# Kernel tuning notes

Measured on AMD Instinct MI355X. Metric: run time of the kernel, lower is better.

## Reference

```python
import jax, jax.numpy as jnp
import numpy as np

B, N, F, H = 2, 2048, 1024, 16
HD = F // H
SQRT_D = float(np.sqrt(F))  # note: module scales by sqrt(in_c), not sqrt(head_dim)


def setup_inputs() -> dict:
    key = jax.random.key(0)
    ks = jax.random.split(key, 9)
    s = 1.0 / np.sqrt(F)
    mk = lambda k: jax.random.uniform(k, (F, F), jnp.float32, -s, s)
    mb = lambda k: jax.random.uniform(k, (F,), jnp.float32, -s, s)
    return {
        "x": jax.random.normal(ks[0], (B, N, F), jnp.float32),
        "Wq": mk(ks[1]), "bq": mb(ks[2]),
        "Wk": mk(ks[3]), "bk": mb(ks[4]),
        "Wv": mk(ks[5]), "bv": mb(ks[6]),
        "Wo": mk(ks[7]), "bo": mb(ks[8]),
    }


def reference(x, Wq, bq, Wk, bk, Wv, bv, Wo, bo):
    b, n, f = x.shape
    # projections (torch Linear: x @ W.T + b); view to (b, n, h, hd)
    q = (x @ Wq.T + bq).reshape(b, n, H, HD)
    k = (x @ Wk.T + bk).reshape(b, n, H, HD)
    v = (x @ Wv.T + bv).reshape(b, n, H, HD)
    score = jnp.einsum('bihd,bjhd->bhij', q, k)
    attn = jax.nn.softmax(score / SQRT_D, axis=-1)
    o = jnp.einsum('bhij,bjhd->bihd', attn, v).reshape(b, n, f)
    return o @ Wo.T + bo
```

## Files before the change

### kernel.cpp

```cpp
#include <hip/hip_runtime.h>
#include <hip/hip_bf16.h>
#include <stdint.h>
#include <stddef.h>

typedef __bf16 bf16;
typedef __attribute__((ext_vector_type(8))) __bf16 bf16x8;
typedef __attribute__((ext_vector_type(4))) __bf16 bf16x4;
typedef __attribute__((ext_vector_type(2))) __bf16 bf16x2;
typedef __attribute__((ext_vector_type(4))) float f32x4;

#define MFMA16(a, b, c) __builtin_amdgcn_mfma_f32_16x16x32_bf16(a, b, c, 0, 0, 0)

#define BB 2
#define SEQ 2048
#define FDIM 1024
#define NH 16
#define HD 64
#define M_TOK 4096
#define N_QKV 3072

#define CSC 0.04508422f

__device__ __forceinline__ void gll16(const bf16* g, bf16* l) {
    __builtin_amdgcn_global_load_lds(
        (const __attribute__((address_space(1))) void*)g,
        (__attribute__((address_space(3))) void*)l, 16, 0, 0);
}

__device__ __forceinline__ bf16 pack_bf16(float f) {
    uint32_t u = __builtin_bit_cast(uint32_t, f);
    uint16_t h = (uint16_t)((u + 0x8000u) >> 16);
    return __builtin_bit_cast(bf16, h);
}

__device__ __forceinline__ uint32_t pk2(float a, float b) {
#if __has_builtin(__builtin_amdgcn_cvt_pk_bf16_f32)
    bf16x2 t = __builtin_amdgcn_cvt_pk_bf16_f32(a, b);
    return __builtin_bit_cast(uint32_t, t);
#else
    uint32_t ua = __builtin_bit_cast(uint32_t, a) + 0x8000u;
    uint32_t ub = __builtin_bit_cast(uint32_t, b) + 0x8000u;
    return __builtin_amdgcn_perm(ub, ua, 0x07060302);
#endif
}

__global__ __launch_bounds__(256) void convert_k(
    const float* __restrict__ x,
    const float* __restrict__ Wq, const float* __restrict__ bq,
    const float* __restrict__ Wk, const float* __restrict__ bk,
    const float* __restrict__ Wv, const float* __restrict__ bv,
    const float* __restrict__ Wo,
    bf16* __restrict__ xb, bf16* __restrict__ Wcat, bf16* __restrict__ Wob,
    float* __restrict__ bcat)
{
    const int tid = blockIdx.x * blockDim.x + threadIdx.x;
    const int nt = gridDim.x * blockDim.x;
    const int NX4 = M_TOK * FDIM / 4;
    const int NW4 = FDIM * FDIM / 4;

    for (int i = tid; i < NX4; i += nt) {
        float4 v = ((const float4*)x)[i];
        bf16x4 o; o[0] = (bf16)v.x; o[1] = (bf16)v.y; o[2] = (bf16)v.z; o[3] = (bf16)v.w;
        ((bf16x4*)xb)[i] = o;
    }
    for (int i = tid; i < NW4; i += nt) {
        float4 v = ((const float4*)Wq)[i];
        bf16x4 o;
        o[0] = (bf16)(v.x * CSC); o[1] = (bf16)(v.y * CSC);
        o[2] = (bf16)(v.z * CSC); o[3] = (bf16)(v.w * CSC);
        ((bf16x4*)Wcat)[i] = o;
        v = ((const float4*)Wk)[i];
        o[0] = (bf16)v.x; o[1] = (bf16)v.y; o[2] = (bf16)v.z; o[3] = (bf16)v.w;
        ((bf16x4*)Wcat)[NW4 + i] = o;
        v = ((const float4*)Wv)[i];
        o[0] = (bf16)v.x; o[1] = (bf16)v.y; o[2] = (bf16)v.z; o[3] = (bf16)v.w;
        ((bf16x4*)Wcat)[2 * NW4 + i] = o;
        v = ((const float4*)Wo)[i];
        o[0] = (bf16)v.x; o[1] = (bf16)v.y; o[2] = (bf16)v.z; o[3] = (bf16)v.w;
        ((bf16x4*)Wob)[i] = o;
    }
    for (int i = tid; i < FDIM; i += nt) {
        bcat[i] = bq[i] * CSC;
        bcat[FDIM + i] = bk[i];
        bcat[2 * FDIM + i] = bv[i];
    }
}

__global__ __launch_bounds__(512, 2) void gemm256(
    const bf16* __restrict__ A,
    const bf16* __restrict__ Bw,
    const float* __restrict__ bias,
    bf16* __restrict__ Cb,
    bf16* __restrict__ VtOut,
    int M, int N, int K)
{
    extern __shared__ char smem[];
    const int tid = threadIdx.x;
    const int lane = tid & 63;
    const int wave = tid >> 6;
    const int wr = wave >> 2;
    const int wc = wave & 3;
    const int m0 = blockIdx.y * 256;
    const int n0 = blockIdx.x * 256;
    const int lrow = lane & 15;
    const int quad = lane >> 4;
    const int NT = K >> 6;

    const int l8 = lane >> 3;
    const int kx = ((lane & 7) ^ l8) << 3;
    const int lcl = wave * 16 + l8;

#define ASTG(sl, kt, mh, c) do { \
    const int _lc = lcl + (c) * 8; \
    const int _gr = m0 + ((_lc >> 6) << 7) + ((mh) << 6) + (_lc & 63); \
    gll16(A + (size_t)_gr * K + (size_t)(kt) * 64 + kx, \
          (bf16*)(smem + (sl) * 65536 + (mh) * 16384 + wave * 2048 + (c) * 1024)); \
} while (0)
#define BSTG(sl, kt, nh, c) do { \
    const int _lc = lcl + (c) * 8; \
    const int _gc = n0 + ((_lc >> 5) << 6) + ((nh) << 5) + (_lc & 31); \
    gll16(Bw + (size_t)_gc * K + (size_t)(kt) * 64 + kx, \
          (bf16*)(smem + (sl) * 65536 + 32768 + (nh) * 16384 + wave * 2048 + (c) * 1024)); \
} while (0)

    const int swz0 = ((quad ^ (lrow & 7)) << 4);
    const int swz1 = (((4 + quad) ^ (lrow & 7)) << 4);
    const int arow = (wr * 64 + lrow) * 128;
    const int brow = (wc * 32 + lrow) * 128;

    f32x4 acc[8][4] = {};
    bf16x8 af[4][2];
    bf16x8 bc[2][2][2];

    ASTG(0, 0, 0, 0); ASTG(0, 0, 0, 1);
    BSTG(0, 0, 0, 0); BSTG(0, 0, 0, 1);
    BSTG(0, 0, 1, 0); BSTG(0, 0, 1, 1);
    ASTG(0, 0, 1, 0); ASTG(0, 0, 1, 1);
    asm volatile("s_waitcnt vmcnt(4)" ::: "memory");
    __builtin_amdgcn_s_barrier();

    for (int t = 0; t < NT; ++t) {
        const int sl = t & 1;
        const int ns = sl ^ 1;
        const char* sb = smem + sl * 65536;
        const bool pf = (t + 1 < NT);

#pragma unroll
        for (int ph = 0; ph < 4; ++ph) {
            const int mh = ph >> 1, nh = ph & 1;
            if (pf) {
                if (ph == 0)      { ASTG(ns, t + 1, 0, 0); ASTG(ns, t + 1, 0, 1); }
                else if (ph == 1) { BSTG(ns, t + 1, 0, 0); BSTG(ns, t + 1, 0, 1); }
                else if (ph == 2) { BSTG(ns, t + 1, 1, 0); BSTG(ns, t + 1, 1, 1); }
                else              { ASTG(ns, t + 1, 1, 0); ASTG(ns, t + 1, 1, 1); }
            }
            if (nh == 0) {
#pragma unroll
                for (int iq = 0; iq < 4; ++iq) {
                    af[iq][0] = *(const bf16x8*)(sb + mh * 16384 + arow + iq * 2048 + swz0);
                    af[iq][1] = *(const bf16x8*)(sb + mh * 16384 + arow + iq * 2048 + swz1);
                }
            }
            if (ph == 0 || ph == 1) {
#pragma unroll
                for (int jq = 0; jq < 2; ++jq) {
                    bc[nh][jq][0] = *(const bf16x8*)(sb + 32768 + nh * 16384 + brow + jq * 2048 + swz0);
                    bc[nh][jq][1] = *(const bf16x8*)(sb + 32768 + nh * 16384 + brow + jq * 2048 + swz1);
                }
            }
            __builtin_amdgcn_s_setprio(1);
#pragma unroll
            for (int iq = 0; iq < 4; ++iq)
#pragma unroll
                for (int jq = 0; jq < 2; ++jq) {
                    acc[mh * 4 + iq][nh * 2 + jq] =
                        MFMA16(af[iq][0], bc[nh][jq][0], acc[mh * 4 + iq][nh * 2 + jq]);
                    acc[mh * 4 + iq][nh * 2 + jq] =
                        MFMA16(af[iq][1], bc[nh][jq][1], acc[mh * 4 + iq][nh * 2 + jq]);
                }
            __builtin_amdgcn_s_setprio(0);
            if (pf) asm volatile("s_waitcnt vmcnt(4)" ::: "memory");
            else    asm volatile("s_waitcnt vmcnt(0)" ::: "memory");
            __builtin_amdgcn_s_barrier();
        }
    }
#undef ASTG
#undef BSTG

    if (VtOut && n0 >= 2048) {
        const int bql = (m0 >> 11);
#pragma unroll
        for (int i = 0; i < 8; ++i) {
#pragma unroll
            for (int j = 0; j < 4; ++j) {
                const int col = n0 + wc * 64 + (j >> 1) * 32 + (j & 1) * 16 + lrow;
                const float bsv = bias[col];
                const int vh = col - 2048;
                const int row = m0 + wr * 128 + (i >> 2) * 64 + (i & 3) * 16 + quad * 4;
                const int jj = row & (SEQ - 1);
                const int g = jj & 63;
                const int jj2 = (jj & ~63) | ((g >> 5) << 5)
                              | (((g >> 2) & 3) << 3) | (((g >> 4) & 1) << 2);
                bf16x4 vv;
#pragma unroll
                for (int r = 0; r < 4; ++r)
                    vv[r] = pack_bf16(acc[i][j][r] + bsv);
                *(bf16x4*)&VtOut[((size_t)bql * 16 * 64 + vh) * SEQ + jj2] = vv;
            }
        }
        return;
    }
#pragma unroll
    for (int i = 0; i < 8; ++i) {
#pragma unroll
        for (int j = 0; j < 4; ++j) {
            const int col = n0 + wc * 64 + (j >> 1) * 32 + (j & 1) * 16 + lrow;
            const float bsv = bias[col];
#pragma unroll
            for (int r = 0; r < 4; ++r) {
                const int row = m0 + wr * 128 + (i >> 2) * 64 + (i & 3) * 16 + quad * 4 + r;
                Cb[(size_t)row * N + col] = pack_bf16(acc[i][j][r] + bsv);
            }
        }
    }
}

__global__ __launch_bounds__(512, 2) void gemm128(
    const bf16* __restrict__ A,
    const bf16* __restrict__ Bw,
    const float* __restrict__ bias,
    float* __restrict__ Cf,
    int M, int N, int K)
{
    extern __shared__ char smem[];
    const int tid = threadIdx.x;
    const int lane = tid & 63;
    const int wave = tid >> 6;
    const int wr = wave >> 2;
    const int wc = wave & 3;
    const int m0 = blockIdx.y * 128;
    const int n0 = blockIdx.x * 128;
    const int lrow = lane & 15;
    const int quad = lane >> 4;
    const int NT = K >> 6;

    const int l8 = lane >> 3;
    const int kx = ((lane & 7) ^ l8) << 3;

#define ASTG(sl, kt, c) do { \
    const int _gr = m0 + (c) * 64 + wave * 8 + l8; \
    gll16(A + (size_t)_gr * K + (size_t)(kt) * 64 + kx, \
          (bf16*)(smem + (sl) * 32768 + (c) * 8192 + wave * 1024)); \
} while (0)
#define BSTG(sl, kt, c) do { \
    const int _gc = n0 + (c) * 64 + wave * 8 + l8; \
    gll16(Bw + (size_t)_gc * K + (size_t)(kt) * 64 + kx, \
          (bf16*)(smem + (sl) * 32768 + 16384 + (c) * 8192 + wave * 1024)); \
} while (0)

    const int swz0 = ((quad ^ (lrow & 7)) << 4);
    const int swz1 = (((4 + quad) ^ (lrow & 7)) << 4);
    const int arow0 = (wr * 32 + lrow) * 128;
    const int brow = (wc * 32 + lrow) * 128;

    f32x4 acc[4][2] = {};
    bf16x8 bfr[2][2];

    BSTG(0, 0, 0); BSTG(0, 0, 1);
    ASTG(0, 0, 0); ASTG(0, 0, 1);
    asm volatile("s_waitcnt vmcnt(1)" ::: "memory");
    __builtin_amdgcn_s_barrier();

    for (int t = 0; t < NT; ++t) {
        const int sl = t & 1;
        const int ns = sl ^ 1;
        const char* sb = smem + sl * 32768;
        const bool pf = (t + 1 < NT);

        if (pf) { BSTG(ns, t + 1, 0); BSTG(ns, t + 1, 1); }
        bf16x8 af[2][2];
#pragma unroll
        for (int jq = 0; jq < 2; ++jq) {
            bfr[jq][0] = *(const bf16x8*)(sb + 16384 + brow + jq * 2048 + swz0);
            bfr[jq][1] = *(const bf16x8*)(sb + 16384 + brow + jq * 2048 + swz1);
        }
#pragma unroll
        for (int iq = 0; iq < 2; ++iq) {
            af[iq][0] = *(const bf16x8*)(sb + arow0 + iq * 2048 + swz0);
            af[iq][1] = *(const bf16x8*)(sb + arow0 + iq * 2048 + swz1);
        }
        __builtin_amdgcn_s_setprio(1);
#pragma unroll
        for (int iq = 0; iq < 2; ++iq)
#pragma unroll
            for (int jq = 0; jq < 2; ++jq) {
                acc[iq][jq] = MFMA16(af[iq][0], bfr[jq][0], acc[iq][jq]);
                acc[iq][jq] = MFMA16(af[iq][1], bfr[jq][1], acc[iq][jq]);
            }
        __builtin_amdgcn_s_setprio(0);
        if (pf) asm volatile("s_waitcnt vmcnt(2)" ::: "memory");
        else    asm volatile("s_waitcnt vmcnt(0)" ::: "memory");
        __builtin_amdgcn_s_barrier();

        if (pf) { ASTG(ns, t + 1, 0); ASTG(ns, t + 1, 1); }
#pragma unroll
        for (int iq = 0; iq < 2; ++iq) {
            af[iq][0] = *(const bf16x8*)(sb + 8192 + arow0 + iq * 2048 + swz0);
            af[iq][1] = *(const bf16x8*)(sb + 8192 + arow0 + iq * 2048 + swz1);
        }
        __builtin_amdgcn_s_setprio(1);
#pragma unroll
        for (int iq = 0; iq < 2; ++iq)
#pragma unroll
            for (int jq = 0; jq < 2; ++jq) {
                acc[2 + iq][jq] = MFMA16(af[iq][0], bfr[jq][0], acc[2 + iq][jq]);
                acc[2 + iq][jq] = MFMA16(af[iq][1], bfr[jq][1], acc[2 + iq][jq]);
            }
        __builtin_amdgcn_s_setprio(0);
        if (pf) asm volatile("s_waitcnt vmcnt(1)" ::: "memory");
        else    asm volatile("s_waitcnt vmcnt(0)" ::: "memory");
        __builtin_amdgcn_s_barrier();
    }
#undef ASTG
#undef BSTG

#pragma unroll
    for (int iq = 0; iq < 4; ++iq) {
#pragma unroll
        for (int jq = 0; jq < 2; ++jq) {
            const int col = n0 + wc * 32 + jq * 16 + lrow;
            const float bsv = bias[col];
#pragma unroll
            for (int r = 0; r < 4; ++r) {
                const int row = m0 + (iq >> 1) * 64 + wr * 32 + (iq & 1) * 16 + quad * 4 + r;
                Cf[(size_t)row * N + col] = acc[iq][jq][r] + bsv;
            }
        }
    }
}

__global__ __launch_bounds__(512, 4) void attn_k(
    const bf16* __restrict__ QKV,
    const bf16* __restrict__ Vt,
    bf16* __restrict__ O)
{
    const int bx = blockIdx.x;
    const int bh = (bx & 7) + 8 * ((bx >> 3) & 3);
    const int qblk = bx >> 5;
    const int b = bh >> 4;
    const int h = bh & 15;
    const int lane = threadIdx.x & 63;
    const int wave = threadIdx.x >> 6;
    const int qg = wave & 3;
    const int jp = wave >> 2;
    const int lrow = lane & 15;
    const int quad = lane >> 4;
    const int lk8 = quad * 8;

    __shared__ __align__(16) bf16 Ks[2][2][128 * 32];
    __shared__ __align__(16) bf16 Vs[2][4][64 * 32];

    const size_t base = (size_t)b * SEQ * N_QKV;
    const bf16* Qp = QKV + base + h * HD;
    const bf16* Kp = QKV + base + FDIM + h * HD;
    const bf16* Vtp = Vt + (size_t)bh * HD * SEQ;

    const int qr0 = qblk * 128 + qg * 32;

    bf16x8 qf[2][2];
#pragma unroll
    for (int qt = 0; qt < 2; ++qt)
#pragma unroll
        for (int ks = 0; ks < 2; ++ks)
            qf[qt][ks] = *(const bf16x8*)(Qp + (size_t)(qr0 + qt * 16 + lrow) * N_QKV
                                          + ks * 32 + lk8);

    bf16x8 ones8;
#pragma unroll
    for (int e = 0; e < 8; ++e) ones8[e] = (bf16)1.0f;

    const f32x4 zf = {0.f, 0.f, 0.f, 0.f};

    f32x4 o[2][4] = {};
    f32x4 o4[2] = {};

    const int srow = wave * 16 + (lane >> 2);
    const int scol = ((lane & 3) ^ ((lane >> 3) & 3)) * 8;
    const bf16* kg = Kp + (size_t)srow * N_QKV + scol;
    const int vsrow = qg * 16 + (lane >> 2);
    const bf16* vg = Vtp + (size_t)vsrow * SEQ + jp * 32 + scol;
    const int kwo = wave * 512;
    const int swz8 = (quad ^ ((lrow >> 1) & 3)) * 8;

    gll16(kg,      &Ks[0][0][0] + kwo);
    gll16(kg + 32, &Ks[0][1][0] + kwo);
    gll16(vg,      &Vs[0][0][0] + kwo);
    gll16(vg + 64, &Vs[0][2][0] + kwo);
    kg += (size_t)128 * N_QKV;
    vg += 128;

    for (int jt = 0; jt < SEQ / 128; ++jt) {
        const int cur = jt & 1;
        __syncthreads();

        if (jt + 1 < SEQ / 128) {
            const int nxt = cur ^ 1;
            gll16(kg,      &Ks[nxt][0][0] + kwo);
            gll16(kg + 32, &Ks[nxt][1][0] + kwo);
            gll16(vg,      &Vs[nxt][0][0] + kwo);
            gll16(vg + 64, &Vs[nxt][2][0] + kwo);
            kg += (size_t)128 * N_QKV;
            vg += 128;
        }

#pragma unroll
        for (int pp = 0; pp < 2; ++pp) {
            const int p = (pp << 1) | jp;
            f32x4 Sp[2][2];
            __builtin_amdgcn_s_setprio(1);
#pragma unroll
            for (int m = 0; m < 2; ++m) {
                const int jn = 2 * p + m;
                bf16x8 kb0 = *(const bf16x8*)&Ks[cur][0][(jn * 16 + lrow) * 32 + swz8];
                bf16x8 kb1 = *(const bf16x8*)&Ks[cur][1][(jn * 16 + lrow) * 32 + swz8];
                Sp[m][0] = MFMA16(kb0, qf[0][0], zf);
                Sp[m][0] = MFMA16(kb1, qf[0][1], Sp[m][0]);
                Sp[m][1] = MFMA16(kb0, qf[1][0], zf);
                Sp[m][1] = MFMA16(kb1, qf[1][1], Sp[m][1]);
            }
            __builtin_amdgcn_s_setprio(0);

            union { bf16x8 v; uint32_t d[4]; } pb[2];
#pragma unroll
            for (int qt = 0; qt < 2; ++qt) {
                const f32x4 s0 = Sp[0][qt];
                const f32x4 s1 = Sp[1][qt];
                pb[qt].d[0] = pk2(__builtin_amdgcn_exp2f(s0[0]),
                                  __builtin_amdgcn_exp2f(s0[1]));
                pb[qt].d[1] = pk2(__builtin_amdgcn_exp2f(s0[2]),
                                  __builtin_amdgcn_exp2f(s0[3]));
                pb[qt].d[2] = pk2(__builtin_amdgcn_exp2f(s1[0]),
                                  __builtin_amdgcn_exp2f(s1[1]));
                pb[qt].d[3] = pk2(__builtin_amdgcn_exp2f(s1[2]),
                                  __builtin_amdgcn_exp2f(s1[3]));
            }

            __builtin_amdgcn_s_setprio(1);
            o4[0] = MFMA16(ones8, pb[0].v, o4[0]);
            o4[1] = MFMA16(ones8, pb[1].v, o4[1]);
#pragma unroll
            for (int df = 0; df < 4; ++df) {
                bf16x8 vA = *(const bf16x8*)&Vs[cur][p][(df * 16 + lrow) * 32 + swz8];
                o[0][df] = MFMA16(vA, pb[0].v, o[0][df]);
                o[1][df] = MFMA16(vA, pb[1].v, o[1][df]);
            }
            __builtin_amdgcn_s_setprio(0);
        }
    }

    __syncthreads();
    float* shO = (float*)Ks;
    float* shS = (float*)Vs;
    if (jp == 1) {
#pragma unroll
        for (int qt = 0; qt < 2; ++qt)
#pragma unroll
            for (int df = 0; df < 4; ++df)
                *(f32x4*)&shO[((((qt * 4 + df) * 4) + qg) * 64 + lane) * 4] = o[qt][df];
        shS[(qg * 64 + lane) * 2 + 0] = o4[0][0];
        shS[(qg * 64 + lane) * 2 + 1] = o4[1][0];
    }
    __syncthreads();
    if (jp == 1) return;

#pragma unroll
    for (int qt = 0; qt < 2; ++qt)
#pragma unroll
        for (int df = 0; df < 4; ++df) {
            f32x4 t = *(const f32x4*)&shO[((((qt * 4 + df) * 4) + qg) * 64 + lane) * 4];
            o[qt][df][0] += t[0]; o[qt][df][1] += t[1];
            o[qt][df][2] += t[2]; o[qt][df][3] += t[3];
        }
    const float den0 = o4[0][0] + shS[(qg * 64 + lane) * 2 + 0];
    const float den1 = o4[1][0] + shS[(qg * 64 + lane) * 2 + 1];

#pragma unroll
    for (int qt = 0; qt < 2; ++qt) {
        const float inv = 1.0f / (qt ? den1 : den0);
        const int q = qr0 + qt * 16 + lrow;
#pragma unroll
        for (int df = 0; df < 4; ++df) {
            bf16x4 vv;
#pragma unroll
            for (int r = 0; r < 4; ++r)
                vv[r] = pack_bf16(o[qt][df][r] * inv);
            *(bf16x4*)&O[(size_t)(b * SEQ + q) * FDIM + h * HD + df * 16 + quad * 4] = vv;
        }
    }
}

extern "C" void kernel_launch(void* const* d_in, const int* in_sizes, int n_in,
                              void* d_out, int out_size, void* d_ws, size_t ws_size,
                              hipStream_t stream) {
    (void)in_sizes; (void)n_in; (void)out_size; (void)ws_size;
    const float* x  = (const float*)d_in[0];
    const float* Wq = (const float*)d_in[1];
    const float* bq = (const float*)d_in[2];
    const float* Wk = (const float*)d_in[3];
    const float* bk = (const float*)d_in[4];
    const float* Wv = (const float*)d_in[5];
    const float* bv = (const float*)d_in[6];
    const float* Wo = (const float*)d_in[7];
    const float* bo = (const float*)d_in[8];
    float* out = (float*)d_out;

    char* ws = (char*)d_ws;
    bf16* xb    = (bf16*)(ws);
    bf16* Wcat  = (bf16*)(ws + 8388608);
    bf16* Wob   = (bf16*)(ws + 14680064);
    float* bcat = (float*)(ws + 16777216);
    bf16* QKV   = (bf16*)(ws + 16789504);
    bf16* Vt    = (bf16*)(ws + 41955328);
    bf16* Ob    = xb;

    static bool s_attr_done = false;
    if (!s_attr_done) {
        (void)hipFuncSetAttribute(reinterpret_cast<const void*>(gemm256),
                                  hipFuncAttributeMaxDynamicSharedMemorySize,
                                  131072);
        (void)hipFuncSetAttribute(reinterpret_cast<const void*>(gemm128),
                                  hipFuncAttributeMaxDynamicSharedMemorySize,
                                  65536);
        s_attr_done = true;
    }

    convert_k<<<dim3(1024), dim3(256), 0, stream>>>(x, Wq, bq, Wk, bk, Wv, bv, Wo,
                                                    xb, Wcat, Wob, bcat);
    gemm256<<<dim3(N_QKV / 256, M_TOK / 256), dim3(512), 131072, stream>>>(
        xb, Wcat, bcat, QKV, Vt, M_TOK, N_QKV, FDIM);
    attn_k<<<dim3((SEQ / 128) * BB * NH), dim3(512), 0, stream>>>(QKV, Vt, Ob);
    gemm128<<<dim3(FDIM / 128, M_TOK / 128), dim3(512), 65536, stream>>>(
        Ob, Wob, bo, out, M_TOK, FDIM, FDIM);
}
```

Baseline: 184.0 us.

## Retile QKV projection GEMM to 256x192 blocks with two-phase pipeline

Changes the QKV GEMM tile from 256x256 to 256x192, giving 16x16=256 blocks instead of 12x16=192. The aim is better coverage of the 256 CUs on MI355X and less wave quantization. Warp layout becomes 4x2 waves, each covering 32 rows by 96 columns per M half. The B fragments are loaded once per k-tile and reused across two A halves, and the loads are restaged in two phases. The Vt-versus-Cb epilogue choice is now made per column, since a 192-wide tile can straddle the V boundary at column 2048, which adds a branch inside the store loop. LDS use drops to 112KB.

```diff
diff --git a/kernel.cpp b/kernel.cpp
--- a/kernel.cpp
+++ b/kernel.cpp
@@ -86,7 +86,7 @@
     }
 }
 
-__global__ __launch_bounds__(512, 2) void gemm256(
+__global__ __launch_bounds__(512, 2) void gemm192(
     const bf16* __restrict__ A,
     const bf16* __restrict__ Bw,
     const float* __restrict__ bias,
@@ -98,128 +98,125 @@
     const int tid = threadIdx.x;
     const int lane = tid & 63;
     const int wave = tid >> 6;
-    const int wr = wave >> 2;
-    const int wc = wave & 3;
+    const int wr = wave >> 1;
+    const int wcn = wave & 1;
     const int m0 = blockIdx.y * 256;
-    const int n0 = blockIdx.x * 256;
+    const int n0 = blockIdx.x * 192;
     const int lrow = lane & 15;
     const int quad = lane >> 4;
     const int NT = K >> 6;
 
     const int l8 = lane >> 3;
     const int kx = ((lane & 7) ^ l8) << 3;
-    const int lcl = wave * 16 + l8;
-
-#define ASTG(sl, kt, mh, c) do { \
-    const int _lc = lcl + (c) * 8; \
-    const int _gr = m0 + ((_lc >> 6) << 7) + ((mh) << 6) + (_lc & 63); \
+
+#define ASTG(sl, kt, c) do { \
+    const int _gr = m0 + (c) * 64 + wave * 8 + l8; \
     gll16(A + (size_t)_gr * K + (size_t)(kt) * 64 + kx, \
-          (bf16*)(smem + (sl) * 65536 + (mh) * 16384 + wave * 2048 + (c) * 1024)); \
+          (bf16*)(smem + (sl) * 57344 + (c) * 8192 + wave * 1024)); \
 } while (0)
-#define BSTG(sl, kt, nh, c) do { \
-    const int _lc = lcl + (c) * 8; \
-    const int _gc = n0 + ((_lc >> 5) << 6) + ((nh) << 5) + (_lc & 31); \
+#define BSTG(sl, kt, c) do { \
+    const int _gc = n0 + (c) * 64 + wave * 8 + l8; \
     gll16(Bw + (size_t)_gc * K + (size_t)(kt) * 64 + kx, \
-          (bf16*)(smem + (sl) * 65536 + 32768 + (nh) * 16384 + wave * 2048 + (c) * 1024)); \
+          (bf16*)(smem + (sl) * 57344 + 32768 + (c) * 8192 + wave * 1024)); \
 } while (0)
 
     const int swz0 = ((quad ^ (lrow & 7)) << 4);
     const int swz1 = (((4 + quad) ^ (lrow & 7)) << 4);
-    const int arow = (wr * 64 + lrow) * 128;
-    const int brow = (wc * 32 + lrow) * 128;
-
-    f32x4 acc[8][4] = {};
-    bf16x8 af[4][2];
-    bf16x8 bc[2][2][2];
-
-    ASTG(0, 0, 0, 0); ASTG(0, 0, 0, 1);
-    BSTG(0, 0, 0, 0); BSTG(0, 0, 0, 1);
-    BSTG(0, 0, 1, 0); BSTG(0, 0, 1, 1);
-    ASTG(0, 0, 1, 0); ASTG(0, 0, 1, 1);
-    asm volatile("s_waitcnt vmcnt(4)" ::: "memory");
+    const int arow0 = (wr * 32 + lrow) * 128;
+    const int brow = (wcn * 96 + lrow) * 128;
+
+    f32x4 acc[2][2][6] = {};
+    bf16x8 bfr[6][2];
+
+    BSTG(0, 0, 0); BSTG(0, 0, 1); BSTG(0, 0, 2);
+    ASTG(0, 0, 0); ASTG(0, 0, 1);
+    ASTG(0, 0, 2); ASTG(0, 0, 3);
+    asm volatile("s_waitcnt vmcnt(2)" ::: "memory");
     __builtin_amdgcn_s_barrier();
 
     for (int t = 0; t < NT; ++t) {
         const int sl = t & 1;
         const int ns = sl ^ 1;
-        const char* sb = smem + sl * 65536;
+        const char* sb = smem + sl * 57344;
         const bool pf = (t + 1 < NT);
 
-#pragma unroll
-        for (int ph = 0; ph < 4; ++ph) {
-            const int mh = ph >> 1, nh = ph & 1;
-            if (pf) {
-                if (ph == 0)      { ASTG(ns, t + 1, 0, 0); ASTG(ns, t + 1, 0, 1); }
-                else if (ph == 1) { BSTG(ns, t + 1, 0, 0); BSTG(ns, t + 1, 0, 1); }
-                else if (ph == 2) { BSTG(ns, t + 1, 1, 0); BSTG(ns, t + 1, 1, 1); }
-                else              { ASTG(ns, t + 1, 1, 0); ASTG(ns, t + 1, 1, 1); }
-            }
-            if (nh == 0) {
-#pragma unroll
-                for (int iq = 0; iq < 4; ++iq) {
-                    af[iq][0] = *(const bf16x8*)(sb + mh * 16384 + arow + iq * 2048 + swz0);
-                    af[iq][1] = *(const bf16x8*)(sb + mh * 16384 + arow + iq * 2048 + swz1);
-                }
-            }
-            if (ph == 0 || ph == 1) {
-#pragma unroll
-                for (int jq = 0; jq < 2; ++jq) {
-                    bc[nh][jq][0] = *(const bf16x8*)(sb + 32768 + nh * 16384 + brow + jq * 2048 + swz0);
-                    bc[nh][jq][1] = *(const bf16x8*)(sb + 32768 + nh * 16384 + brow + jq * 2048 + swz1);
-                }
-            }
-            __builtin_amdgcn_s_setprio(1);
-#pragma unroll
-            for (int iq = 0; iq < 4; ++iq)
-#pragma unroll
-                for (int jq = 0; jq < 2; ++jq) {
-                    acc[mh * 4 + iq][nh * 2 + jq] =
-                        MFMA16(af[iq][0], bc[nh][jq][0], acc[mh * 4 + iq][nh * 2 + jq]);
-                    acc[mh * 4 + iq][nh * 2 + jq] =
-                        MFMA16(af[iq][1], bc[nh][jq][1], acc[mh * 4 + iq][nh * 2 + jq]);
-                }
-            __builtin_amdgcn_s_setprio(0);
-            if (pf) asm volatile("s_waitcnt vmcnt(4)" ::: "memory");
-            else    asm volatile("s_waitcnt vmcnt(0)" ::: "memory");
-            __builtin_amdgcn_s_barrier();
-        }
+        if (pf) {
+            BSTG(ns, t + 1, 0); BSTG(ns, t + 1, 1); BSTG(ns, t + 1, 2);
+            ASTG(ns, t + 1, 0); ASTG(ns, t + 1, 1);
+        }
+        bf16x8 af[2][2];
+#pragma unroll
+        for (int jf = 0; jf < 6; ++jf) {
+            bfr[jf][0] = *(const bf16x8*)(sb + 32768 + brow + jf * 2048 + swz0);
+            bfr[jf][1] = *(const bf16x8*)(sb + 32768 + brow + jf * 2048 + swz1);
+        }
+#pragma unroll
+        for (int f = 0; f < 2; ++f) {
+            af[f][0] = *(const bf16x8*)(sb + arow0 + f * 2048 + swz0);
+            af[f][1] = *(const bf16x8*)(sb + arow0 + f * 2048 + swz1);
+        }
+        __builtin_amdgcn_s_setprio(1);
+#pragma unroll
+        for (int f = 0; f < 2; ++f)
+#pragma unroll
+            for (int jf = 0; jf < 6; ++jf) {
+                acc[0][f][jf] = MFMA16(af[f][0], bfr[jf][0], acc[0][f][jf]);
+                acc[0][f][jf] = MFMA16(af[f][1], bfr[jf][1], acc[0][f][jf]);
+            }
+        __builtin_amdgcn_s_setprio(0);
+        if (pf) asm volatile("s_waitcnt vmcnt(5)" ::: "memory");
+        else    asm volatile("s_waitcnt vmcnt(0)" ::: "memory");
+        __builtin_amdgcn_s_barrier();
+
+        if (pf) { ASTG(ns, t + 1, 2); ASTG(ns, t + 1, 3); }
+#pragma unroll
+        for (int f = 0; f < 2; ++f) {
+            af[f][0] = *(const bf16x8*)(sb + 16384 + arow0 + f * 2048 + swz0);
+            af[f][1] = *(const bf16x8*)(sb + 16384 + arow0 + f * 2048 + swz1);
+        }
+        __builtin_amdgcn_s_setprio(1);
+#pragma unroll
+        for (int f = 0; f < 2; ++f)
+#pragma unroll
+            for (int jf = 0; jf < 6; ++jf) {
+                acc[1][f][jf] = MFMA16(af[f][0], bfr[jf][0], acc[1][f][jf]);
+                acc[1][f][jf] = MFMA16(af[f][1], bfr[jf][1], acc[1][f][jf]);
+            }
+        __builtin_amdgcn_s_setprio(0);
+        if (pf) asm volatile("s_waitcnt vmcnt(2)" ::: "memory");
+        else    asm volatile("s_waitcnt vmcnt(0)" ::: "memory");
+        __builtin_amdgcn_s_barrier();
     }
 #undef ASTG
 #undef BSTG
 
-    if (VtOut && n0 >= 2048) {
-        const int bql = (m0 >> 11);
-#pragma unroll
-        for (int i = 0; i < 8; ++i) {
-#pragma unroll
-            for (int j = 0; j < 4; ++j) {
-                const int col = n0 + wc * 64 + (j >> 1) * 32 + (j & 1) * 16 + lrow;
+    const int bql = (m0 >> 11);
+#pragma unroll
+    for (int mh = 0; mh < 2; ++mh) {
+#pragma unroll
+        for (int f = 0; f < 2; ++f) {
+#pragma unroll
+            for (int jf = 0; jf < 6; ++jf) {
+                const int col = n0 + wcn * 96 + jf * 16 + lrow;
                 const float bsv = bias[col];
-                const int vh = col - 2048;
-                const int row = m0 + wr * 128 + (i >> 2) * 64 + (i & 3) * 16 + quad * 4;
-                const int jj = row & (SEQ - 1);
-                const int g = jj & 63;
-                const int jj2 = (jj & ~63) | ((g >> 5) << 5)
-                              | (((g >> 2) & 3) << 3) | (((g >> 4) & 1) << 2);
-                bf16x4 vv;
-#pragma unroll
-                for (int r = 0; r < 4; ++r)
-                    vv[r] = pack_bf16(acc[i][j][r] + bsv);
-                *(bf16x4*)&VtOut[((size_t)bql * 16 * 64 + vh) * SEQ + jj2] = vv;
-            }
-        }
-        return;
-    }
-#pragma unroll
-    for (int i = 0; i < 8; ++i) {
-#pragma unroll
-        for (int j = 0; j < 4; ++j) {
-            const int col = n0 + wc * 64 + (j >> 1) * 32 + (j & 1) * 16 + lrow;
-            const float bsv = bias[col];
-#pragma unroll
-            for (int r = 0; r < 4; ++r) {
-                const int row = m0 + wr * 128 + (i >> 2) * 64 + (i & 3) * 16 + quad * 4 + r;
-                Cb[(size_t)row * N + col] = pack_bf16(acc[i][j][r] + bsv);
+                const int row = m0 + mh * 128 + wr * 32 + f * 16 + quad * 4;
+                if (VtOut && col >= 2048) {
+                    const int vh = col - 2048;
+                    const int jj = row & (SEQ - 1);
+                    const int g = jj & 63;
+                    const int jj2 = (jj & ~63) | ((g >> 5) << 5)
+                                  | (((g >> 2) & 3) << 3) | (((g >> 4) & 1) << 2);
+                    bf16x4 vv;
+#pragma unroll
+                    for (int r = 0; r < 4; ++r)
+                        vv[r] = pack_bf16(acc[mh][f][jf][r] + bsv);
+                    *(bf16x4*)&VtOut[((size_t)bql * 16 * 64 + vh) * SEQ + jj2] = vv;
+                } else {
+#pragma unroll
+                    for (int r = 0; r < 4; ++r)
+                        Cb[(size_t)(row + r) * N + col] =
+                            pack_bf16(acc[mh][f][jf][r] + bsv);
+                }
             }
         }
     }
@@ -525,9 +522,9 @@
 
     static bool s_attr_done = false;
     if (!s_attr_done) {
-        (void)hipFuncSetAttribute(reinterpret_cast<const void*>(gemm256),
+        (void)hipFuncSetAttribute(reinterpret_cast<const void*>(gemm192),
                                   hipFuncAttributeMaxDynamicSharedMemorySize,
-                                  131072);
+                                  114688);
         (void)hipFuncSetAttribute(reinterpret_cast<const void*>(gemm128),
                                   hipFuncAttributeMaxDynamicSharedMemorySize,
                                   65536);
@@ -536,7 +533,7 @@
 
     convert_k<<<dim3(1024), dim3(256), 0, stream>>>(x, Wq, bq, Wk, bk, Wv, bv, Wo,
                                                     xb, Wcat, Wob, bcat);
-    gemm256<<<dim3(N_QKV / 256, M_TOK / 256), dim3(512), 131072, stream>>>(
+    gemm192<<<dim3(N_QKV / 192, M_TOK / 256), dim3(512), 114688, stream>>>(
         xb, Wcat, bcat, QKV, Vt, M_TOK, N_QKV, FDIM);
     attn_k<<<dim3((SEQ / 128) * BB * NH), dim3(512), 0, stream>>>(QKV, Vt, Ob);
     gemm128<<<dim3(FDIM / 128, M_TOK / 128), dim3(512), 65536, stream>>>(
```

After: 180.7 us (median of 2 runs). About the same (-1.8%).

## Restructure QKV GEMM: XCD-aware block remap, new wave tiling and staging schedule

Applied to the files above, without the earlier changes.

The QKV projection GEMM now launches on a 1D grid and remaps block IDs so that consecutive blocks (which interleave across the eight XCDs) land on tiles sharing A/B panels within each XCD's L2. Each wave now holds all four B fragments for its 64-column strip once per k-tile and streams A fragments in four phases, which cuts LDS B re-reads. Global-to-LDS staging is regrouped into larger A-quarter and B-half loads, with adjusted vmcnt waits, an extra barrier and an lgkmcnt wait before the MFMAs. The extra barrier per phase adds synchronisation cost, and the output row/column mapping had to change to match the new accumulator layout.

```diff
diff --git a/kernel.cpp b/kernel.cpp
--- a/kernel.cpp
+++ b/kernel.cpp
@@ -86,7 +86,7 @@
     }
 }
 
-__global__ __launch_bounds__(512, 2) void gemm256(
+__global__ __launch_bounds__(512, 2) void gemm_qkv(
     const bf16* __restrict__ A,
     const bf16* __restrict__ Bw,
     const float* __restrict__ bias,
@@ -100,43 +100,35 @@
     const int wave = tid >> 6;
     const int wr = wave >> 2;
     const int wc = wave & 3;
-    const int m0 = blockIdx.y * 256;
-    const int n0 = blockIdx.x * 256;
+    const int lin = (blockIdx.x & 7) * 24 + (blockIdx.x >> 3);
+    const int m0 = (lin / 12) * 256;
+    const int n0 = (lin % 12) * 256;
     const int lrow = lane & 15;
     const int quad = lane >> 4;
     const int NT = K >> 6;
 
     const int l8 = lane >> 3;
     const int kx = ((lane & 7) ^ l8) << 3;
-    const int lcl = wave * 16 + l8;
-
-#define ASTG(sl, kt, mh, c) do { \
-    const int _lc = lcl + (c) * 8; \
-    const int _gr = m0 + ((_lc >> 6) << 7) + ((mh) << 6) + (_lc & 63); \
-    gll16(A + (size_t)_gr * K + (size_t)(kt) * 64 + kx, \
-          (bf16*)(smem + (sl) * 65536 + (mh) * 16384 + wave * 2048 + (c) * 1024)); \
-} while (0)
-#define BSTG(sl, kt, nh, c) do { \
-    const int _lc = lcl + (c) * 8; \
-    const int _gc = n0 + ((_lc >> 5) << 6) + ((nh) << 5) + (_lc & 31); \
-    gll16(Bw + (size_t)_gc * K + (size_t)(kt) * 64 + kx, \
-          (bf16*)(smem + (sl) * 65536 + 32768 + (nh) * 16384 + wave * 2048 + (c) * 1024)); \
-} while (0)
+
+#define AQ(sl, kt, q) gll16(A + (size_t)(m0 + (q) * 64 + wave * 8 + l8) * K \
+        + (size_t)(kt) * 64 + kx, \
+        (bf16*)(smem + (sl) * 65536 + (q) * 8192 + wave * 1024))
+#define BH(sl, kt, h, c) gll16(Bw + (size_t)(n0 + (h) * 128 + wave * 16 + (c) * 8 + l8) * K \
+        + (size_t)(kt) * 64 + kx, \
+        (bf16*)(smem + (sl) * 65536 + 32768 + (h) * 16384 + wave * 2048 + (c) * 1024))
 
     const int swz0 = ((quad ^ (lrow & 7)) << 4);
     const int swz1 = (((4 + quad) ^ (lrow & 7)) << 4);
-    const int arow = (wr * 64 + lrow) * 128;
-    const int brow = (wc * 32 + lrow) * 128;
+    const int abase = (wr * 2) * 8192 + lrow * 128;
+    const int bbase = 32768 + (wc >> 1) * 16384 + ((wc & 1) * 64 + lrow) * 128;
 
     f32x4 acc[8][4] = {};
-    bf16x8 af[4][2];
-    bf16x8 bc[2][2][2];
-
-    ASTG(0, 0, 0, 0); ASTG(0, 0, 0, 1);
-    BSTG(0, 0, 0, 0); BSTG(0, 0, 0, 1);
-    BSTG(0, 0, 1, 0); BSTG(0, 0, 1, 1);
-    ASTG(0, 0, 1, 0); ASTG(0, 0, 1, 1);
-    asm volatile("s_waitcnt vmcnt(4)" ::: "memory");
+    bf16x8 bfr[4][2];
+
+    AQ(0, 0, 0); AQ(0, 0, 2);
+    BH(0, 0, 0, 0); BH(0, 0, 0, 1); BH(0, 0, 1, 0); BH(0, 0, 1, 1);
+    AQ(0, 0, 1); AQ(0, 0, 3);
+    asm volatile("s_waitcnt vmcnt(2)" ::: "memory");
     __builtin_amdgcn_s_barrier();
 
     for (int t = 0; t < NT; ++t) {
@@ -146,46 +138,50 @@
         const bool pf = (t + 1 < NT);
 
 #pragma unroll
-        for (int ph = 0; ph < 4; ++ph) {
-            const int mh = ph >> 1, nh = ph & 1;
+        for (int p = 0; p < 4; ++p) {
+            bf16x8 af[2][2];
+            const int aoff = abase + (p >> 1) * 8192 + (p & 1) * 4096;
+            af[0][0] = *(const bf16x8*)(sb + aoff + swz0);
+            af[0][1] = *(const bf16x8*)(sb + aoff + swz1);
+            af[1][0] = *(const bf16x8*)(sb + aoff + 2048 + swz0);
+            af[1][1] = *(const bf16x8*)(sb + aoff + 2048 + swz1);
+            if (p == 0) {
+#pragma unroll
+                for (int jq = 0; jq < 4; ++jq) {
+                    bfr[jq][0] = *(const bf16x8*)(sb + bbase + jq * 2048 + swz0);
+                    bfr[jq][1] = *(const bf16x8*)(sb + bbase + jq * 2048 + swz1);
+                }
+            }
             if (pf) {
-                if (ph == 0)      { ASTG(ns, t + 1, 0, 0); ASTG(ns, t + 1, 0, 1); }
-                else if (ph == 1) { BSTG(ns, t + 1, 0, 0); BSTG(ns, t + 1, 0, 1); }
-                else if (ph == 2) { BSTG(ns, t + 1, 1, 0); BSTG(ns, t + 1, 1, 1); }
-                else              { ASTG(ns, t + 1, 1, 0); ASTG(ns, t + 1, 1, 1); }
-            }
-            if (nh == 0) {
-#pragma unroll
-                for (int iq = 0; iq < 4; ++iq) {
-                    af[iq][0] = *(const bf16x8*)(sb + mh * 16384 + arow + iq * 2048 + swz0);
-                    af[iq][1] = *(const bf16x8*)(sb + mh * 16384 + arow + iq * 2048 + swz1);
-                }
-            }
-            if (ph == 0 || ph == 1) {
-#pragma unroll
-                for (int jq = 0; jq < 2; ++jq) {
-                    bc[nh][jq][0] = *(const bf16x8*)(sb + 32768 + nh * 16384 + brow + jq * 2048 + swz0);
-                    bc[nh][jq][1] = *(const bf16x8*)(sb + 32768 + nh * 16384 + brow + jq * 2048 + swz1);
-                }
-            }
+                if (p == 0)      { AQ(ns, t + 1, 0); AQ(ns, t + 1, 2); }
+                else if (p == 1) { BH(ns, t + 1, 0, 0); BH(ns, t + 1, 0, 1);
+                                   BH(ns, t + 1, 1, 0); BH(ns, t + 1, 1, 1); }
+                else if (p == 2) { AQ(ns, t + 1, 1); AQ(ns, t + 1, 3); }
+            }
+            __builtin_amdgcn_s_barrier();
+            asm volatile("s_waitcnt lgkmcnt(0)" ::: "memory");
+            __builtin_amdgcn_sched_barrier(0);
             __builtin_amdgcn_s_setprio(1);
 #pragma unroll
-            for (int iq = 0; iq < 4; ++iq)
-#pragma unroll
-                for (int jq = 0; jq < 2; ++jq) {
-                    acc[mh * 4 + iq][nh * 2 + jq] =
-                        MFMA16(af[iq][0], bc[nh][jq][0], acc[mh * 4 + iq][nh * 2 + jq]);
-                    acc[mh * 4 + iq][nh * 2 + jq] =
-                        MFMA16(af[iq][1], bc[nh][jq][1], acc[mh * 4 + iq][nh * 2 + jq]);
+            for (int f = 0; f < 2; ++f)
+#pragma unroll
+                for (int jq = 0; jq < 4; ++jq) {
+                    acc[2 * p + f][jq] = MFMA16(af[f][0], bfr[jq][0], acc[2 * p + f][jq]);
+                    acc[2 * p + f][jq] = MFMA16(af[f][1], bfr[jq][1], acc[2 * p + f][jq]);
                 }
             __builtin_amdgcn_s_setprio(0);
-            if (pf) asm volatile("s_waitcnt vmcnt(4)" ::: "memory");
-            else    asm volatile("s_waitcnt vmcnt(0)" ::: "memory");
+            if (p == 1) {
+                if (pf) asm volatile("s_waitcnt vmcnt(6)" ::: "memory");
+                else    asm volatile("s_waitcnt vmcnt(0)" ::: "memory");
+            } else if (p == 3) {
+                if (pf) asm volatile("s_waitcnt vmcnt(2)" ::: "memory");
+                else    asm volatile("s_waitcnt vmcnt(0)" ::: "memory");
+            }
             __builtin_amdgcn_s_barrier();
         }
     }
-#undef ASTG
-#undef BSTG
+#undef AQ
+#undef BH
 
     if (VtOut && n0 >= 2048) {
         const int bql = (m0 >> 11);
@@ -193,10 +189,10 @@
         for (int i = 0; i < 8; ++i) {
 #pragma unroll
             for (int j = 0; j < 4; ++j) {
-                const int col = n0 + wc * 64 + (j >> 1) * 32 + (j & 1) * 16 + lrow;
+                const int col = n0 + wc * 64 + j * 16 + lrow;
                 const float bsv = bias[col];
                 const int vh = col - 2048;
-                const int row = m0 + wr * 128 + (i >> 2) * 64 + (i & 3) * 16 + quad * 4;
+                const int row = m0 + wr * 128 + (i >> 1) * 32 + (i & 1) * 16 + quad * 4;
                 const int jj = row & (SEQ - 1);
                 const int g = jj & 63;
                 const int jj2 = (jj & ~63) | ((g >> 5) << 5)
@@ -214,11 +210,11 @@
     for (int i = 0; i < 8; ++i) {
 #pragma unroll
         for (int j = 0; j < 4; ++j) {
-            const int col = n0 + wc * 64 + (j >> 1) * 32 + (j & 1) * 16 + lrow;
+            const int col = n0 + wc * 64 + j * 16 + lrow;
             const float bsv = bias[col];
 #pragma unroll
             for (int r = 0; r < 4; ++r) {
-                const int row = m0 + wr * 128 + (i >> 2) * 64 + (i & 3) * 16 + quad * 4 + r;
+                const int row = m0 + wr * 128 + (i >> 1) * 32 + (i & 1) * 16 + quad * 4 + r;
                 Cb[(size_t)row * N + col] = pack_bf16(acc[i][j][r] + bsv);
             }
         }
@@ -525,7 +521,7 @@
 
     static bool s_attr_done = false;
     if (!s_attr_done) {
-        (void)hipFuncSetAttribute(reinterpret_cast<const void*>(gemm256),
+        (void)hipFuncSetAttribute(reinterpret_cast<const void*>(gemm_qkv),
                                   hipFuncAttributeMaxDynamicSharedMemorySize,
                                   131072);
         (void)hipFuncSetAttribute(reinterpret_cast<const void*>(gemm128),
@@ -536,7 +532,7 @@
 
     convert_k<<<dim3(1024), dim3(256), 0, stream>>>(x, Wq, bq, Wk, bk, Wv, bv, Wo,
                                                     xb, Wcat, Wob, bcat);
-    gemm256<<<dim3(N_QKV / 256, M_TOK / 256), dim3(512), 131072, stream>>>(
+    gemm_qkv<<<dim3((N_QKV / 256) * (M_TOK / 256)), dim3(512), 131072, stream>>>(
         xb, Wcat, bcat, QKV, Vt, M_TOK, N_QKV, FDIM);
     attn_k<<<dim3((SEQ / 128) * BB * NH), dim3(512), 0, stream>>>(QKV, Vt, Ob);
     gemm128<<<dim3(FDIM / 128, M_TOK / 128), dim3(512), 65536, stream>>>(
```

New measurement: 182.8 us. About the same (-0.6%).
